# Optimization experiments

Measured on AMD Instinct MI355X. Metric: run time of the kernel, lower is better.

The kernel has to match this reference:

```python
import jax, jax.numpy as jnp
import numpy as np

N = 100000      # nodes (== batch_size)
E = 1600000     # edges (avg degree 16)
D_IN = 64
D_H = 64
D_OUT = 17


def setup_inputs() -> dict:
    key = jax.random.key(0)
    ks = jax.random.split(key, 18)
    inp = {
        "x": jax.random.normal(ks[0], (N, D_IN), dtype=jnp.float32),
        "edge_index": jax.random.randint(ks[1], (2, E), 0, N, dtype=jnp.int32).astype(jnp.int64),
    }
    dims = [(D_IN, D_H), (D_H, D_H), (D_H, D_H), (D_H, D_H), (D_H, D_OUT)]
    k = 2
    for i, (di, do) in enumerate(dims, start=1):
        scale = 1.0 / np.sqrt(di)
        inp[f"Wl{i}"] = jax.random.uniform(ks[k], (di, do), jnp.float32, -scale, scale); k += 1
        inp[f"bl{i}"] = jnp.zeros((do,), jnp.float32)
        inp[f"Wr{i}"] = jax.random.uniform(ks[k], (di, do), jnp.float32, -scale, scale); k += 1
    return inp


def _sage_conv(x, src, dst, Wl, bl, Wr):
    # PyG SAGEConv (mean aggr): out[i] = mean_{j in N(i)} x[j] @ Wl + bl + x[i] @ Wr
    msg_sum = jax.ops.segment_sum(x[src], dst, num_segments=N)          # [N, d]
    deg = jax.ops.segment_sum(jnp.ones((src.shape[0],), x.dtype), dst, num_segments=N)
    agg = msg_sum / jnp.maximum(deg, 1.0)[:, None]
    return agg @ Wl + bl + x @ Wr


def reference(x, edge_index, Wl1, bl1, Wr1, Wl2, bl2, Wr2, Wl3, bl3, Wr3,
              Wl4, bl4, Wr4, Wl5, bl5, Wr5):
    src, dst = edge_index[0], edge_index[1]
    h = jax.nn.relu(_sage_conv(x, src, dst, Wl1, bl1, Wr1))
    h = jax.nn.relu(_sage_conv(h, src, dst, Wl2, bl2, Wr2))
    h = jax.nn.relu(_sage_conv(h, src, dst, Wl3, bl3, Wr3))
    h = jax.nn.relu(_sage_conv(h, src, dst, Wl4, bl4, Wr4))
    h = jax.nn.relu(_sage_conv(h, src, dst, Wl5, bl5, Wr5))
    return h.reshape(N, 17)  # x.view(batch_size, 17)
```

## Files before the change

### kernel.cpp

```cpp
#include <hip/hip_runtime.h>

#define NN 100000
#define NE 1600000
constexpr int NBLK = (NN + 255) / 256;

typedef _Float16 half8 __attribute__((ext_vector_type(8)));

__global__ void k_detect(const unsigned int* __restrict__ ei32, int* __restrict__ flag) {
    if (threadIdx.x == 0 && blockIdx.x == 0) {
        unsigned int acc = 0;
#pragma unroll
        for (int i = 1; i < 16; i += 2) acc |= ei32[i];
        *flag = (acc == 0) ? 1 : 0;
    }
}


__global__ __launch_bounds__(256) void k_deg(const void* __restrict__ eiraw,
                                             const int* __restrict__ flag,
                                             int* __restrict__ deg) {
    int e = blockIdx.x * 256 + threadIdx.x;
    if (e >= NE) return;
    int dst;
    if (*flag) dst = (int)((const long long*)eiraw)[(size_t)NE + e];
    else       dst = ((const int*)eiraw)[(size_t)NE + e];
    if ((unsigned)dst < (unsigned)NN) atomicAdd(&deg[dst], 1);
}

__global__ __launch_bounds__(256) void k_scan1(const int* __restrict__ deg,
                                               int* __restrict__ bsum) {
    __shared__ int sh[256];
    int t = threadIdx.x;
    int i = blockIdx.x * 256 + t;
    sh[t] = (i < NN) ? deg[i] : 0;
    __syncthreads();
    for (int off = 128; off > 0; off >>= 1) {
        if (t < off) sh[t] += sh[t + off];
        __syncthreads();
    }
    if (t == 0) bsum[blockIdx.x] = sh[0];
}

__global__ __launch_bounds__(512) void k_scan2(const int* __restrict__ bsum,
                                               int* __restrict__ bscan) {
    __shared__ int sh[512];
    int t = threadIdx.x;
    sh[t] = (t < NBLK) ? bsum[t] : 0;
    __syncthreads();
    for (int off = 1; off < 512; off <<= 1) {
        int a = (t >= off) ? sh[t - off] : 0;
        __syncthreads();
        sh[t] += a;
        __syncthreads();
    }
    if (t < NBLK) bscan[t] = (t == 0) ? 0 : sh[t - 1];
}

__global__ __launch_bounds__(256) void k_scan3(const int* __restrict__ deg,
                                               const int* __restrict__ bscan,
                                               int* __restrict__ row_start) {
    __shared__ int sh[256];
    int t = threadIdx.x;
    int i = blockIdx.x * 256 + t;
    int v = (i < NN) ? deg[i] : 0;
    sh[t] = v;
    __syncthreads();
    for (int off = 1; off < 256; off <<= 1) {
        int a = (t >= off) ? sh[t - off] : 0;
        __syncthreads();
        sh[t] += a;
        __syncthreads();
    }
    if (i < NN) row_start[i] = bscan[blockIdx.x] + sh[t] - v;
}

__global__ __launch_bounds__(256) void k_init(const int* __restrict__ deg,
                                              const int* __restrict__ row_start,
                                              float* __restrict__ inv_deg,
                                              int* __restrict__ cursor) {
    int i = blockIdx.x * 256 + threadIdx.x;
    if (i < NN) {
        int d = deg[i];
        inv_deg[i] = 1.0f / (float)(d > 0 ? d : 1);
        cursor[i] = row_start[i];
    }
}

__global__ __launch_bounds__(256) void k_fill(const void* __restrict__ eiraw,
                                              const int* __restrict__ flag,
                                              int* __restrict__ cursor,
                                              int* __restrict__ csr_src) {
    int e = blockIdx.x * 256 + threadIdx.x;
    if (e >= NE) return;
    int src, dst;
    if (*flag) {
        src = (int)((const long long*)eiraw)[e];
        dst = (int)((const long long*)eiraw)[(size_t)NE + e];
    } else {
        src = ((const int*)eiraw)[e];
        dst = ((const int*)eiraw)[(size_t)NE + e];
    }
    if ((unsigned)dst < (unsigned)NN) {
        int pos = atomicAdd(&cursor[dst], 1);
        int sv = ((unsigned)src < (unsigned)NN) ? src : 0;
        __builtin_nontemporal_store(sv, &csr_src[pos]);
    }
}


__global__ __launch_bounds__(256) void k_gemm64(const float* x,
                                                const float* __restrict__ Wl,
                                                const float* __restrict__ Wr,
                                                const float* __restrict__ bl,
                                                _Float16* __restrict__ y,
                                                float* z) {
    __shared__ float sXT[64][68];
    __shared__ float sW[64][132];
    int t = threadIdx.x;
    int row0 = blockIdx.x * 64;

    for (int idx = t; idx < 64 * 64; idx += 256) {
        int k = idx >> 6, c = idx & 63;
        sW[k][c] = Wl[idx];
        sW[k][64 + c] = Wr[idx];
    }
    for (int idx = t; idx < 64 * 64; idx += 256) {
        int r = idx >> 6, k = idx & 63;
        int gr = row0 + r;
        sXT[k][r] = (gr < NN) ? x[(size_t)gr * 64 + k] : 0.f;
    }
    __syncthreads();

    int cg = t & 15;
    int rg = t >> 4;
    int r0 = rg * 4, c0 = cg * 8;
    float acc[4][8];
#pragma unroll
    for (int i = 0; i < 4; i++)
#pragma unroll
        for (int j = 0; j < 8; j++) acc[i][j] = 0.f;

    for (int k = 0; k < 64; k++) {
        float xv[4], wv[8];
#pragma unroll
        for (int i = 0; i < 4; i++) xv[i] = sXT[k][r0 + i];
#pragma unroll
        for (int j = 0; j < 8; j++) wv[j] = sW[k][c0 + j];
#pragma unroll
        for (int i = 0; i < 4; i++)
#pragma unroll
            for (int j = 0; j < 8; j++) acc[i][j] += xv[i] * wv[j];
    }

#pragma unroll
    for (int i = 0; i < 4; i++) {
        int gr = row0 + r0 + i;
        if (gr < NN) {
            if (cg < 8) {
                half8 hv;
#pragma unroll
                for (int j = 0; j < 8; j++) hv[j] = (_Float16)acc[i][j];
                *reinterpret_cast<half8*>(&y[(size_t)gr * 64 + c0]) = hv;
            } else {
                int zc = c0 - 64;
#pragma unroll
                for (int j = 0; j < 8; j++)
                    z[(size_t)gr * 64 + zc + j] = acc[i][j] + bl[zc + j];
            }
        }
    }
}

__global__ __launch_bounds__(256) void k_gemm17(const float* __restrict__ x,
                                                const float* __restrict__ Wl,
                                                const float* __restrict__ Wr,
                                                const float* __restrict__ bl,
                                                float* __restrict__ y,
                                                float* __restrict__ z) {
    __shared__ float sW[2][64][17];
    __shared__ float sX[128][65];
    int t = threadIdx.x;
    int row0 = blockIdx.x * 128;

    for (int idx = t; idx < 64 * 17; idx += 256) {
        sW[0][idx / 17][idx % 17] = Wl[idx];
        sW[1][idx / 17][idx % 17] = Wr[idx];
    }
    for (int idx = t; idx < 128 * 64; idx += 256) {
        int r = idx >> 6, k = idx & 63;
        int gr = row0 + r;
        sX[r][k] = (gr < NN) ? x[(size_t)gr * 64 + k] : 0.f;
    }
    __syncthreads();

    int row = t & 127;
    int mat = t >> 7;
    float acc[17];
#pragma unroll
    for (int j = 0; j < 17; j++) acc[j] = 0.f;

    for (int k = 0; k < 64; k++) {
        float xv = sX[row][k];
#pragma unroll
        for (int j = 0; j < 17; j++) acc[j] += xv * sW[mat][k][j];
    }

    int gr = row0 + row;
    if (gr < NN) {
        if (mat == 0) {
#pragma unroll
            for (int j = 0; j < 17; j++) y[(size_t)gr * 17 + j] = acc[j];
        } else {
#pragma unroll
            for (int j = 0; j < 17; j++) z[(size_t)gr * 17 + j] = acc[j] + bl[j];
        }
    }
}


template <int DO, typename T>
__global__ __launch_bounds__(256) void k_gather(const T* __restrict__ y,
                                                const int* __restrict__ csr_src,
                                                const int* __restrict__ row_start,
                                                const int* __restrict__ degv,
                                                const float* __restrict__ inv_deg,
                                                float* __restrict__ io) {
    int gw = (blockIdx.x * 256 + threadIdx.x) >> 6;
    if (gw >= NN) return;
    int lane = threadIdx.x & 63;
    int ch = (lane < DO) ? lane : 0;
    const T* yc = y + ch;
    int s = row_start[gw];
    int d = degv[gw];
    float a0 = 0.f, a1 = 0.f, a2 = 0.f, a3 = 0.f;

    for (int base = 0; base < d; base += 64) {
        int nk = min(d - base, 64);
        int srcv = csr_src[s + base + ((lane < nk) ? lane : 0)];
        int k = 0;
        for (; k + 4 <= nk; k += 4) {
            int s0 = __shfl(srcv, k, 64);
            int s1 = __shfl(srcv, k + 1, 64);
            int s2 = __shfl(srcv, k + 2, 64);
            int s3 = __shfl(srcv, k + 3, 64);
            a0 += (float)yc[(size_t)s0 * DO];
            a1 += (float)yc[(size_t)s1 * DO];
            a2 += (float)yc[(size_t)s2 * DO];
            a3 += (float)yc[(size_t)s3 * DO];
        }
        for (; k < nk; k++) {
            int s0 = __shfl(srcv, k, 64);
            a0 += (float)yc[(size_t)s0 * DO];
        }
    }

    if (lane < DO) {
        float v = ((a0 + a1) + (a2 + a3)) * inv_deg[gw] + io[(size_t)gw * DO + lane];
        io[(size_t)gw * DO + lane] = fmaxf(v, 0.f);
    }
}

__global__ __launch_bounds__(256) void k_zero_out(float* __restrict__ out, int n) {
    int i = blockIdx.x * 256 + threadIdx.x;
    if (i < n) out[i] = 0.f;
}


extern "C" void kernel_launch(void* const* d_in, const int* in_sizes, int n_in,
                              void* d_out, int out_size, void* d_ws, size_t ws_size,
                              hipStream_t stream) {
    (void)in_sizes; (void)n_in;
    const float* x0 = (const float*)d_in[0];
    const void* ei = d_in[1];
    const float *Wl[5], *bl[5], *Wr[5];
    for (int l = 0; l < 5; l++) {
        Wl[l] = (const float*)d_in[2 + 3 * l];
        bl[l] = (const float*)d_in[3 + 3 * l];
        Wr[l] = (const float*)d_in[4 + 3 * l];
    }

    char* w = (char*)d_ws;
    size_t off = 0;
    auto carve = [&](size_t bytes) {
        void* p = w + off;
        off += (bytes + 255) & ~(size_t)255;
        return p;
    };
    int* eiflag    = (int*)carve(256);
    int* deg       = (int*)carve((size_t)NN * 4);
    int* row_start = (int*)carve((size_t)NN * 4);
    int* cursor    = (int*)carve((size_t)NN * 4);
    float* inv_deg = (float*)carve((size_t)NN * 4);
    int* bsum      = (int*)carve(512 * 4);
    int* bscan     = (int*)carve(512 * 4);
    int* csr_src   = (int*)carve((size_t)NE * 4);
    void* ybuf     = carve((size_t)NN * 64 * 4);
    float* hA      = (float*)carve((size_t)NN * 64 * 4);
    _Float16* yh   = (_Float16*)ybuf;
    float* y17     = (float*)ybuf;

    if (off > ws_size) {
        k_zero_out<<<(out_size + 255) / 256, 256, 0, stream>>>((float*)d_out, out_size);
        return;
    }

    k_detect<<<1, 64, 0, stream>>>((const unsigned int*)ei, eiflag);
    hipMemsetAsync(deg, 0, (size_t)NN * 4, stream);
    const int egrid = (NE + 255) / 256;
    k_deg<<<egrid, 256, 0, stream>>>(ei, eiflag, deg);
    k_scan1<<<NBLK, 256, 0, stream>>>(deg, bsum);
    k_scan2<<<1, 512, 0, stream>>>(bsum, bscan);
    k_scan3<<<NBLK, 256, 0, stream>>>(deg, bscan, row_start);
    k_init<<<NBLK, 256, 0, stream>>>(deg, row_start, inv_deg, cursor);
    k_fill<<<egrid, 256, 0, stream>>>(ei, eiflag, cursor, csr_src);

    const int ggrid = (NN * 64) / 256;
    const int mgrid = (NN + 63) / 64;

    k_gemm64<<<mgrid, 256, 0, stream>>>(x0, Wl[0], Wr[0], bl[0], yh, hA);
    k_gather<64, _Float16><<<ggrid, 256, 0, stream>>>(yh, csr_src, row_start, deg, inv_deg, hA);
    for (int l = 1; l < 4; l++) {
        k_gemm64<<<mgrid, 256, 0, stream>>>(hA, Wl[l], Wr[l], bl[l], yh, hA);
        k_gather<64, _Float16><<<ggrid, 256, 0, stream>>>(yh, csr_src, row_start, deg, inv_deg, hA);
    }
    float* outp = (float*)d_out;
    k_gemm17<<<(NN + 127) / 128, 256, 0, stream>>>(hA, Wl[4], Wr[4], bl[4], y17, outp);
    k_gather<17, float><<<ggrid, 256, 0, stream>>>(y17, csr_src, row_start, deg, inv_deg, outp);
}
```

Baseline: 771.8 us.

## Split CSR fill into dst-range passes and unroll gather loop by eight

The CSR fill kernel now runs as seven passes. Each pass handles only edges whose destination falls in one 16K-node range, so the atomic cursor updates and csr_src writes stay in a smaller, cache-resident region. The cost is reading the dst array seven times and launching seven kernels. Separately, the gather loop is unrolled to eight independent accumulators so more loads are in flight per wave, at the cost of more registers.

```diff
diff --git a/kernel.cpp b/kernel.cpp
--- a/kernel.cpp
+++ b/kernel.cpp
@@ -3,6 +3,7 @@
 #define NN 100000
 #define NE 1600000
 constexpr int NBLK = (NN + 255) / 256;
+#define NPASS 7
 
 typedef _Float16 half8 __attribute__((ext_vector_type(8)));
 
@@ -86,25 +87,22 @@
     }
 }
 
-__global__ __launch_bounds__(256) void k_fill(const void* __restrict__ eiraw,
-                                              const int* __restrict__ flag,
-                                              int* __restrict__ cursor,
-                                              int* __restrict__ csr_src) {
+__global__ __launch_bounds__(256) void k_fill_part(const void* __restrict__ eiraw,
+                                                   const int* __restrict__ flag,
+                                                   int* __restrict__ cursor,
+                                                   int* __restrict__ csr_src,
+                                                   int pass) {
     int e = blockIdx.x * 256 + threadIdx.x;
     if (e >= NE) return;
-    int src, dst;
-    if (*flag) {
-        src = (int)((const long long*)eiraw)[e];
-        dst = (int)((const long long*)eiraw)[(size_t)NE + e];
-    } else {
-        src = ((const int*)eiraw)[e];
-        dst = ((const int*)eiraw)[(size_t)NE + e];
-    }
-    if ((unsigned)dst < (unsigned)NN) {
-        int pos = atomicAdd(&cursor[dst], 1);
-        int sv = ((unsigned)src < (unsigned)NN) ? src : 0;
-        __builtin_nontemporal_store(sv, &csr_src[pos]);
-    }
+    int dst;
+    if (*flag) dst = (int)((const long long*)eiraw)[(size_t)NE + e];
+    else       dst = ((const int*)eiraw)[(size_t)NE + e];
+    if ((unsigned)dst >= (unsigned)NN || (dst >> 14) != pass) return;
+    int src;
+    if (*flag) src = (int)((const long long*)eiraw)[e];
+    else       src = ((const int*)eiraw)[e];
+    int pos = atomicAdd(&cursor[dst], 1);
+    csr_src[pos] = ((unsigned)src < (unsigned)NN) ? src : 0;
 }
 
 
@@ -232,30 +230,30 @@
     const T* yc = y + ch;
     int s = row_start[gw];
     int d = degv[gw];
-    float a0 = 0.f, a1 = 0.f, a2 = 0.f, a3 = 0.f;
+    float a[8];
+#pragma unroll
+    for (int j = 0; j < 8; j++) a[j] = 0.f;
 
     for (int base = 0; base < d; base += 64) {
         int nk = min(d - base, 64);
         int srcv = csr_src[s + base + ((lane < nk) ? lane : 0)];
         int k = 0;
-        for (; k + 4 <= nk; k += 4) {
-            int s0 = __shfl(srcv, k, 64);
-            int s1 = __shfl(srcv, k + 1, 64);
-            int s2 = __shfl(srcv, k + 2, 64);
-            int s3 = __shfl(srcv, k + 3, 64);
-            a0 += (float)yc[(size_t)s0 * DO];
-            a1 += (float)yc[(size_t)s1 * DO];
-            a2 += (float)yc[(size_t)s2 * DO];
-            a3 += (float)yc[(size_t)s3 * DO];
+        for (; k + 8 <= nk; k += 8) {
+            int si[8];
+#pragma unroll
+            for (int j = 0; j < 8; j++) si[j] = __shfl(srcv, k + j, 64);
+#pragma unroll
+            for (int j = 0; j < 8; j++) a[j] += (float)yc[(size_t)si[j] * DO];
         }
         for (; k < nk; k++) {
             int s0 = __shfl(srcv, k, 64);
-            a0 += (float)yc[(size_t)s0 * DO];
+            a[0] += (float)yc[(size_t)s0 * DO];
         }
     }
 
     if (lane < DO) {
-        float v = ((a0 + a1) + (a2 + a3)) * inv_deg[gw] + io[(size_t)gw * DO + lane];
+        float sum = ((a[0] + a[1]) + (a[2] + a[3])) + ((a[4] + a[5]) + (a[6] + a[7]));
+        float v = sum * inv_deg[gw] + io[(size_t)gw * DO + lane];
         io[(size_t)gw * DO + lane] = fmaxf(v, 0.f);
     }
 }
@@ -312,7 +310,8 @@
     k_scan2<<<1, 512, 0, stream>>>(bsum, bscan);
     k_scan3<<<NBLK, 256, 0, stream>>>(deg, bscan, row_start);
     k_init<<<NBLK, 256, 0, stream>>>(deg, row_start, inv_deg, cursor);
-    k_fill<<<egrid, 256, 0, stream>>>(ei, eiflag, cursor, csr_src);
+    for (int p = 0; p < NPASS; p++)
+        k_fill_part<<<egrid, 256, 0, stream>>>(ei, eiflag, cursor, csr_src, p);
 
     const int ggrid = (NN * 64) / 256;
     const int mgrid = (NN + 63) / 64;
```

Measured after the change: 757.0 us. No clear change (-1.9%).
